# Kernel tuning notes

Hardware: AMD Instinct MI355X
Metric: run time of the kernel (lower is better)

## Reference

```python
import jax, jax.numpy as jnp
import numpy as np

B, L, DH = 4, 4096, 1024
T, DG = 1024, 768
P = 256


def setup_inputs() -> dict:
    key = jax.random.key(0)
    k1, k2, k3, k4, k5 = jax.random.split(key, 5)
    H = jax.random.normal(k1, (B, L, DH), dtype=jnp.float32)
    G = jax.random.normal(k2, (B, T, DG), dtype=jnp.float32)
    # key mask: True = padded/masked. Guarantee at least one valid key per row.
    mask = jax.random.randint(k3, (B, L), 0, 2).astype(jnp.bool_)
    mask = mask.at[:, 0].set(False)
    # torch Linear weights: [out, in]
    Wk_w = jax.random.normal(k4, (P, DH), dtype=jnp.float32) * (DH ** -0.5)
    Wq_w = jax.random.normal(k5, (P, DG), dtype=jnp.float32) * (DG ** -0.5)
    return {"H": H, "G": G, "mask": mask, "Wk_w": Wk_w, "Wq_w": Wq_w}


def reference(H, G, mask, Wk_w, Wq_w):
    # K = Wk(H): [B,L,P]; Q = Wq(G): [B,T,P]
    K = jnp.einsum('bld,pd->blp', H, Wk_w)
    Q = jnp.einsum('btd,pd->btp', G, Wq_w)
    scale = P ** -0.5
    logits = jnp.einsum('btp,blp->btl', Q, K) * scale  # [B,T,L]
    neg_inf = jnp.finfo(logits.dtype).min
    logits = jnp.where(mask[:, None, :], neg_inf, logits)
    alpha = jax.nn.softmax(logits, axis=-1)  # softmax over L (streaming-equivalent)
    Z = jnp.einsum('btl,bld->btd', alpha, H)  # [B,T,DH]
    return Z
```

## Files before the change

### kernel.cpp

```cpp
#include <hip/hip_runtime.h>
#include <hip/hip_bf16.h>


typedef __attribute__((ext_vector_type(8))) short short8;
typedef __attribute__((ext_vector_type(4))) float f32x4;

static __device__ __forceinline__ unsigned short bf16bits(float x) {
    __hip_bfloat16 b = __float2bfloat16(x);
    return *(unsigned short*)&b;
}

static __device__ __forceinline__ void gload_lds16(const __hip_bfloat16* g,
                                                   __hip_bfloat16* l)
{
    auto gp = (const __attribute__((address_space(1))) unsigned int*)(uintptr_t)g;
    auto lp = (__attribute__((address_space(3))) unsigned int*)(unsigned int)(uintptr_t)l;
    __builtin_amdgcn_global_load_lds(gp, lp, 16, 0, 0);
}

__global__ __launch_bounds__(256)
void cvt_f32_bf16_kernel(const float* __restrict__ in,
                         unsigned short* __restrict__ out, int n4)
{
    const int i = blockIdx.x * 256 + threadIdx.x;
    if (i >= n4) return;
    float4 v = ((const float4*)in)[i];
    ushort4 o;
    o.x = bf16bits(v.x); o.y = bf16bits(v.y);
    o.z = bf16bits(v.z); o.w = bf16bits(v.w);
    ((ushort4*)out)[i] = o;
}

__global__ __launch_bounds__(256)
void h_prep_kernel(const float* __restrict__ H,
                   __hip_bfloat16* __restrict__ Hbf,
                   __hip_bfloat16* __restrict__ Ht, int L, int D)
{
    const long b = blockIdx.z;
    const float* Hb = H + b * (long)L * D;
    __hip_bfloat16* Hbfb = Hbf + b * (long)L * D;
    __hip_bfloat16* Htb  = Ht  + b * (long)D * L;
    __shared__ __align__(16) __hip_bfloat16 tile[64][72];
    const int l0 = blockIdx.x * 64, d0 = blockIdx.y * 64;
    const int tx = threadIdx.x & 15, ty = threadIdx.x >> 4;
    #pragma unroll
    for (int p = 0; p < 4; ++p) {
        const int row = ty + p * 16;
        const float4 v = *(const float4*)(&Hb[(long)(l0 + row) * D + d0 + tx * 4]);
        ushort4 o;
        o.x = bf16bits(v.x); o.y = bf16bits(v.y);
        o.z = bf16bits(v.z); o.w = bf16bits(v.w);
        *(ushort4*)(&Hbfb[(long)(l0 + row) * D + d0 + tx * 4]) = o;
        tile[tx * 4 + 0][row] = __float2bfloat16(v.x);
        tile[tx * 4 + 1][row] = __float2bfloat16(v.y);
        tile[tx * 4 + 2][row] = __float2bfloat16(v.z);
        tile[tx * 4 + 3][row] = __float2bfloat16(v.w);
    }
    __syncthreads();
    const int ll = threadIdx.x & 7;
    const int dq = threadIdx.x >> 3;
    #pragma unroll
    for (int q = 0; q < 2; ++q) {
        const int dd = dq + q * 32;
        const short8 v = *(const short8*)(&tile[dd][ll * 8]);
        *(short8*)(&Htb[(long)(d0 + dd) * L + l0 + ll * 8]) = v;
    }
}

template <typename OutT, int SPLITK, int MODE>
__global__ __launch_bounds__(256)
void gemm_bt_kernel(const __hip_bfloat16* __restrict__ A,
                    const __hip_bfloat16* __restrict__ Bm,
                    OutT* __restrict__ C,
                    int K, int lda, int ldb, int ldc,
                    long batchStrideA, long batchStrideB, long batchStrideC,
                    float scale,
                    const unsigned char* __restrict__ mask,
                    const int* __restrict__ widthPtr,
                    float* __restrict__ rowsum,
                    int rowsumStride,
                    long partStride)
{
    int bx = blockIdx.x, by = blockIdx.y, bz = blockIdx.z;
    {
        const int nwg = gridDim.x * gridDim.y * gridDim.z;
        if ((nwg & 7) == 0) {
            int lin = bx + gridDim.x * (by + gridDim.y * bz);
            lin = (lin & 7) * (nwg >> 3) + (lin >> 3);
            bx = lin % gridDim.x;
            const int t = lin / gridDim.x;
            by = t % gridDim.y;
            bz = t / gridDim.y;
        }
    }

    const int zb = bz / SPLITK;
    const int kc = bz % SPLITK;
    A  += (long)zb * batchStrideA;
    Bm += (long)zb * batchStrideB;
    C  += (long)zb * batchStrideC + (long)kc * partStride;
    const int Kloc  = K / SPLITK;
    const int kbase = kc * Kloc;
    const int NT    = Kloc / 32;

    const int tid  = threadIdx.x;
    const int lane = tid & 63;
    const int wave = tid >> 6;
    const int wm = (wave & 1) * 64;
    const int wn = (wave >> 1) * 64;
    const int rowBase = bx * 128;
    const int colBase = by * 128;

    __shared__ __align__(16) __hip_bfloat16 lds_pool[24576];
    __hip_bfloat16* AsP = lds_pool;
    __hip_bfloat16* BsP = lds_pool + 12288;

    f32x4 acc[4][4];
    #pragma unroll
    for (int i = 0; i < 4; ++i)
        #pragma unroll
        for (int j = 0; j < 4; ++j)
            acc[i][j] = (f32x4){0.f, 0.f, 0.f, 0.f};

    const int srow = lane >> 2;
    const int scol = ((lane & 3) ^ ((lane >> 3) & 3)) * 8;
    const long ar0 = (long)(rowBase + wave * 32 + srow) * lda;
    const long ar1 = ar0 + 16l * lda;
    const long br0 = (long)(colBase + wave * 32 + srow) * ldb;
    const long br1 = br0 + 16l * ldb;

    const int mrow = lane & 15;
    const int koff = (((lane >> 4) ^ ((lane >> 1) & 3)) * 8);

    auto stage = [&](int buf, int t) {
        const int kk = kbase + t * 32 + scol;
        gload_lds16(A  + ar0 + kk, AsP + buf * 4096 + wave * 1024);
        gload_lds16(A  + ar1 + kk, AsP + buf * 4096 + wave * 1024 + 512);
        gload_lds16(Bm + br0 + kk, BsP + buf * 4096 + wave * 1024);
        gload_lds16(Bm + br1 + kk, BsP + buf * 4096 + wave * 1024 + 512);
    };

    stage(0, 0);
    if (NT > 1) stage(1, 1);

    int cur = 0;
    for (int t = 0; t < NT; ++t) {
        if (t + 1 < NT)
            asm volatile("s_waitcnt vmcnt(4)" ::: "memory");
        else
            asm volatile("s_waitcnt vmcnt(0)" ::: "memory");
        __builtin_amdgcn_s_barrier();
        if (t + 2 < NT) {
            const int nxt2 = (cur >= 1) ? cur - 1 : cur + 2;
            stage(nxt2, t + 2);
        }

        short8 af[4], bf[4];
        #pragma unroll
        for (int mi = 0; mi < 4; ++mi)
            af[mi] = *(const short8*)(AsP + cur * 4096 + (wm + mi * 16 + mrow) * 32 + koff);
        #pragma unroll
        for (int ni = 0; ni < 4; ++ni)
            bf[ni] = *(const short8*)(BsP + cur * 4096 + (wn + ni * 16 + mrow) * 32 + koff);

        #pragma unroll
        for (int mi = 0; mi < 4; ++mi)
            #pragma unroll
            for (int ni = 0; ni < 4; ++ni)
                acc[mi][ni] = __builtin_amdgcn_mfma_f32_16x16x32_bf16(
                    af[mi], bf[ni], acc[mi][ni], 0, 0, 0);
        cur = (cur == 2) ? 0 : cur + 1;
    }

    const int crow0 = (lane >> 4) * 4;
    const int ccol  = lane & 15;

    if constexpr (MODE == 2 || sizeof(OutT) == 2) {
        __syncthreads();
        __hip_bfloat16* cst = lds_pool;

        if constexpr (MODE == 2) {
            const int w = *widthPtr;
            const long mbase = (long)zb * ldc;
            bool mk[4];
            #pragma unroll
            for (int ni = 0; ni < 4; ++ni) {
                const long midx = mbase + colBase + wn + ni * 16 + ccol;
                if (w == 1)      mk[ni] = mask[midx] != 0;
                else if (w == 2) mk[ni] = ((const unsigned short*)mask)[midx] != 0;
                else if (w == 4) mk[ni] = ((const unsigned int*)mask)[midx] != 0;
                else { uint2 q = ((const uint2*)mask)[midx]; mk[ni] = (q.x | q.y) != 0; }
            }
            #pragma unroll
            for (int mi = 0; mi < 4; ++mi) {
                #pragma unroll
                for (int r = 0; r < 4; ++r) {
                    const int row = wm + mi * 16 + crow0 + r;
                    float rs = 0.f;
                    #pragma unroll
                    for (int ni = 0; ni < 4; ++ni) {
                        const int col = wn + ni * 16 + ccol;
                        const float e = mk[ni] ? 0.f
                                               : __expf(acc[mi][ni][r] * scale);
                        const __hip_bfloat16 pb = __float2bfloat16(e);
                        cst[row * 136 + (((col >> 3) ^ (row >> 3)) << 3) + (col & 7)] = pb;
                        rs += __bfloat162float(pb);
                    }
                    rs += __shfl_xor(rs, 1, 64);
                    rs += __shfl_xor(rs, 2, 64);
                    rs += __shfl_xor(rs, 4, 64);
                    rs += __shfl_xor(rs, 8, 64);
                    if ((lane & 15) == 0)
                        atomicAdd(&rowsum[(long)zb * rowsumStride + rowBase + row], rs);
                }
            }
        } else {
            #pragma unroll
            for (int mi = 0; mi < 4; ++mi) {
                #pragma unroll
                for (int ni = 0; ni < 4; ++ni) {
                    #pragma unroll
                    for (int r = 0; r < 4; ++r) {
                        const int row = wm + mi * 16 + crow0 + r;
                        const int col = wn + ni * 16 + ccol;
                        cst[row * 136 + (((col >> 3) ^ (row >> 3)) << 3) + (col & 7)] =
                            __float2bfloat16(acc[mi][ni][r] * scale);
                    }
                }
            }
        }
        __syncthreads();
        const int g   = tid & 15;
        const int r4  = tid >> 4;
        const int lof = ((g ^ r4) << 3);
        #pragma unroll
        for (int k = 0; k < 8; ++k) {
            const int row = r4 * 8 + k;
            const short8 v = *(const short8*)(cst + row * 136 + lof);
            *(short8*)(&((__hip_bfloat16*)C)[(long)(rowBase + row) * ldc + colBase + g * 8]) = v;
        }
    } else {
        #pragma unroll
        for (int mi = 0; mi < 4; ++mi) {
            #pragma unroll
            for (int ni = 0; ni < 4; ++ni) {
                #pragma unroll
                for (int r = 0; r < 4; ++r) {
                    const int row = rowBase + wm + mi * 16 + crow0 + r;
                    const int col = colBase + wn + ni * 16 + ccol;
                    ((float*)C)[(long)row * ldc + col] = acc[mi][ni][r] * scale;
                }
            }
        }
    }
}

__global__ __launch_bounds__(256)
void combine_kernel(const float* __restrict__ Zp,
                    const float* __restrict__ rowsum,
                    float* __restrict__ Z, long partStride)
{
    const int i = blockIdx.x * 256 + threadIdx.x;
    const float4 a = ((const float4*)Zp)[i];
    const float4 b = ((const float4*)(Zp + partStride))[i];
    const float inv = 1.0f / rowsum[i >> 8];
    float4 o;
    o.x = (a.x + b.x) * inv;
    o.y = (a.y + b.y) * inv;
    o.z = (a.z + b.z) * inv;
    o.w = (a.w + b.w) * inv;
    ((float4*)Z)[i] = o;
}

__global__ __launch_bounds__(256)
void mask_width_kernel(const unsigned char* __restrict__ m, int* __restrict__ widthOut)
{
    __shared__ int c1, c2, c4, c8, cp;
    if (threadIdx.x == 0) { c1 = c2 = c4 = c8 = cp = 0; }
    __syncthreads();
    int l1 = 0, l2 = 0, l4 = 0, l8 = 0, lp = 0;
    const unsigned short* m16 = (const unsigned short*)m;
    const unsigned int*   m32 = (const unsigned int*)m;
    for (int i = threadIdx.x; i < 16384; i += 256) l1 += (m[i] != 0);
    for (int i = threadIdx.x; i < 8192;  i += 256) {
        l2 += (m16[i] != 0);
        lp += ((m[2 * i] != 0) == (m[2 * i + 1] != 0));
    }
    for (int i = threadIdx.x; i < 4096;  i += 256) l4 += (m32[i] != 0);
    for (int i = threadIdx.x; i < 2048;  i += 256) l8 += ((m32[2 * i] | m32[2 * i + 1]) != 0);
    atomicAdd(&c1, l1); atomicAdd(&c2, l2); atomicAdd(&c4, l4);
    atomicAdd(&c8, l8); atomicAdd(&cp, lp);
    __syncthreads();
    if (threadIdx.x == 0) {
        const float f1 = fabsf(c1 / 16384.f - 0.5f);
        const float f2 = fabsf(c2 / 8192.f  - 0.5f);
        const float f4 = fabsf(c4 / 4096.f  - 0.5f);
        const float f8 = fabsf(c8 / 2048.f  - 0.5f);
        int w = 1; float best = f1;
        if (f2 < best) { best = f2; w = 2; }
        if (f4 < best) { best = f4; w = 4; }
        if (f8 < best) { best = f8; w = 8; }
        if (w == 1 && cp > 7400) w = 2;
        *widthOut = w;
    }
}

extern "C" void kernel_launch(void* const* d_in, const int* in_sizes, int n_in,
                              void* d_out, int out_size, void* d_ws, size_t ws_size,
                              hipStream_t stream)
{
    constexpr int B = 4, L = 4096, DH = 1024, T = 1024, DG = 768, P = 256;

    const float* H  = (const float*)d_in[0];
    const float* G  = (const float*)d_in[1];
    const void*  mask = d_in[2];
    const float* Wk = (const float*)d_in[3];
    const float* Wq = (const float*)d_in[4];
    for (int i = 0; i < n_in; ++i) {
        switch (in_sizes[i]) {
            case B * L * DH: H    = (const float*)d_in[i]; break;
            case B * T * DG: G    = (const float*)d_in[i]; break;
            case B * L:      mask = d_in[i];               break;
            case P * DH:     Wk   = (const float*)d_in[i]; break;
            case P * DG:     Wq   = (const float*)d_in[i]; break;
        }
    }
    float* Z = (float*)d_out;

    char* ws = (char*)d_ws;
    __hip_bfloat16* Hbf  = (__hip_bfloat16*)ws;
    float*          Zp   = (float*)ws;
    __hip_bfloat16* Ht   = (__hip_bfloat16*)(ws + (32l << 20));
    __hip_bfloat16* Gbf  = (__hip_bfloat16*)(ws + (64l << 20));
    __hip_bfloat16* Qbf  = (__hip_bfloat16*)(ws + (70l << 20));
    __hip_bfloat16* Kbf  = (__hip_bfloat16*)(ws + (72l << 20));
    __hip_bfloat16* Wkbf = (__hip_bfloat16*)(ws + (80l << 20));
    __hip_bfloat16* Wqbf = (__hip_bfloat16*)(ws + (80l << 20) + (512l << 10));
    float*          rowsum    = (float*)(ws + (80l << 20) + (896l << 10));
    int*            widthFlag = (int*)  (ws + (80l << 20) + (960l << 10));
    __hip_bfloat16* Sb   = (__hip_bfloat16*)(ws + (81l << 20));

    constexpr long ZPART = (long)B * T * DH;

    const dim3 blk(256);

    hipMemsetAsync(rowsum, 0, (size_t)(B * T) * sizeof(float), stream);

    mask_width_kernel<<<dim3(1), blk, 0, stream>>>((const unsigned char*)mask, widthFlag);

    h_prep_kernel<<<dim3(L / 64, DH / 64, B), blk, 0, stream>>>(H, Hbf, Ht, L, DH);
    cvt_f32_bf16_kernel<<<dim3((P * DH) / 1024), blk, 0, stream>>>(Wk, (unsigned short*)Wkbf, (P * DH) / 4);
    cvt_f32_bf16_kernel<<<dim3((P * DG) / 1024), blk, 0, stream>>>(Wq, (unsigned short*)Wqbf, (P * DG) / 4);
    cvt_f32_bf16_kernel<<<dim3((B * T * DG) / 1024), blk, 0, stream>>>(G, (unsigned short*)Gbf, (B * T * DG) / 4);

    gemm_bt_kernel<__hip_bfloat16, 1, 0><<<dim3((B * T) / 128, P / 128, 1), blk, 0, stream>>>(
        Gbf, Wqbf, Qbf, DG, DG, DG, P, 0, 0, 0, 1.0f,
        nullptr, nullptr, nullptr, 0, 0);
    gemm_bt_kernel<__hip_bfloat16, 1, 0><<<dim3((B * L) / 128, P / 128, 1), blk, 0, stream>>>(
        Hbf, Wkbf, Kbf, DH, DH, DH, P, 0, 0, 0, 1.0f,
        nullptr, nullptr, nullptr, 0, 0);
    gemm_bt_kernel<__hip_bfloat16, 1, 2><<<dim3(T / 128, L / 128, B), blk, 0, stream>>>(
        Qbf, Kbf, Sb, P, P, P, L,
        (long)T * P, (long)L * P, (long)T * L, 0.0625f,
        (const unsigned char*)mask, widthFlag, rowsum, T, 0);
    gemm_bt_kernel<float, 2, 0><<<dim3(T / 128, DH / 128, B * 2), blk, 0, stream>>>(
        Sb, Ht, Zp, L, L, L, DH,
        (long)T * L, (long)DH * L, (long)T * DH, 1.0f,
        nullptr, nullptr, nullptr, 0, ZPART);
    combine_kernel<<<dim3((B * T * DH / 4) / 256), blk, 0, stream>>>(
        Zp, rowsum, Z, ZPART);
}
```

Before: 254.6 us.

## Compact unmasked keys per batch and skip masked work in all GEMMs

Adds a mask scan kernel that builds, for each batch, a compacted list of unmasked key indices and a padded count. H is gathered into compacted bf16 and transposed buffers, and the K projection, QK^T/exp and alpha*H GEMMs skip tiles or shorten K past the padded valid count. With about half the keys masked, this roughly halves the work on the large L dimension. The cost is an extra scan launch, gathered loads in h_prep, and dependence on runtime counts. Split-K chunking now depends on lcpad being divisible by 64.

```diff
diff --git a/kernel.cpp b/kernel.cpp
--- a/kernel.cpp
+++ b/kernel.cpp
@@ -32,25 +32,118 @@
 }
 
 __global__ __launch_bounds__(256)
+void mask_width_kernel(const unsigned char* __restrict__ m, int* __restrict__ widthOut)
+{
+    __shared__ int c1, c2, c4, c8, cp;
+    if (threadIdx.x == 0) { c1 = c2 = c4 = c8 = cp = 0; }
+    __syncthreads();
+    int l1 = 0, l2 = 0, l4 = 0, l8 = 0, lp = 0;
+    const unsigned short* m16 = (const unsigned short*)m;
+    const unsigned int*   m32 = (const unsigned int*)m;
+    for (int i = threadIdx.x; i < 16384; i += 256) l1 += (m[i] != 0);
+    for (int i = threadIdx.x; i < 8192;  i += 256) {
+        l2 += (m16[i] != 0);
+        lp += ((m[2 * i] != 0) == (m[2 * i + 1] != 0));
+    }
+    for (int i = threadIdx.x; i < 4096;  i += 256) l4 += (m32[i] != 0);
+    for (int i = threadIdx.x; i < 2048;  i += 256) l8 += ((m32[2 * i] | m32[2 * i + 1]) != 0);
+    atomicAdd(&c1, l1); atomicAdd(&c2, l2); atomicAdd(&c4, l4);
+    atomicAdd(&c8, l8); atomicAdd(&cp, lp);
+    __syncthreads();
+    if (threadIdx.x == 0) {
+        const float f1 = fabsf(c1 / 16384.f - 0.5f);
+        const float f2 = fabsf(c2 / 8192.f  - 0.5f);
+        const float f4 = fabsf(c4 / 4096.f  - 0.5f);
+        const float f8 = fabsf(c8 / 2048.f  - 0.5f);
+        int w = 1; float best = f1;
+        if (f2 < best) { best = f2; w = 2; }
+        if (f4 < best) { best = f4; w = 4; }
+        if (f8 < best) { best = f8; w = 8; }
+        if (w == 1 && cp > 7400) w = 2;
+        *widthOut = w;
+    }
+}
+
+__global__ __launch_bounds__(256)
+void mask_scan_kernel(const void* __restrict__ mask, const int* __restrict__ widthPtr,
+                      unsigned short* __restrict__ idx,
+                      int* __restrict__ lc, int* __restrict__ lcpad, int L)
+{
+    const int b = blockIdx.x;
+    const int tid = threadIdx.x;
+    const int w = *widthPtr;
+    const unsigned char*  m8  = (const unsigned char*)mask;
+    const unsigned short* m16 = (const unsigned short*)mask;
+    const unsigned int*   m32 = (const unsigned int*)mask;
+    const uint2*          m64 = (const uint2*)mask;
+
+    bool v[16];
+    int cnt = 0;
+    #pragma unroll
+    for (int i = 0; i < 16; ++i) {
+        const int l = tid * 16 + i;
+        const long mi = (long)b * L + l;
+        bool masked;
+        if (w == 1)      masked = m8[mi] != 0;
+        else if (w == 2) masked = m16[mi] != 0;
+        else if (w == 4) masked = m32[mi] != 0;
+        else             { uint2 q = m64[mi]; masked = (q.x | q.y) != 0; }
+        v[i] = !masked;
+        cnt += v[i] ? 1 : 0;
+    }
+    __shared__ int waveTot[4];
+    int pre = cnt;
+    #pragma unroll
+    for (int off = 1; off < 64; off <<= 1) {
+        const int t = __shfl_up(pre, off, 64);
+        if ((tid & 63) >= off) pre += t;
+    }
+    if ((tid & 63) == 63) waveTot[tid >> 6] = pre;
+    __syncthreads();
+    int waveOff = 0;
+    for (int wv = 0; wv < (tid >> 6); ++wv) waveOff += waveTot[wv];
+    int o = waveOff + pre - cnt;
+    #pragma unroll
+    for (int i = 0; i < 16; ++i)
+        if (v[i]) idx[(long)b * L + (o++)] = (unsigned short)(tid * 16 + i);
+    if (tid == 255) {
+        const int total = waveOff + pre;
+        lc[b] = total;
+        lcpad[b] = (total + 127) & ~127;
+    }
+}
+
+__global__ __launch_bounds__(256)
 void h_prep_kernel(const float* __restrict__ H,
                    __hip_bfloat16* __restrict__ Hbf,
-                   __hip_bfloat16* __restrict__ Ht, int L, int D)
-{
-    const long b = blockIdx.z;
-    const float* Hb = H + b * (long)L * D;
-    __hip_bfloat16* Hbfb = Hbf + b * (long)L * D;
-    __hip_bfloat16* Htb  = Ht  + b * (long)D * L;
+                   __hip_bfloat16* __restrict__ Ht,
+                   const unsigned short* __restrict__ idx,
+                   const int* __restrict__ lc, const int* __restrict__ lcpad,
+                   int L, int D)
+{
+    const int b = blockIdx.z;
+    const int c0 = blockIdx.x * 64;
+    if (c0 >= lcpad[b]) return;
+    const int Lcb = lc[b];
+    const float* Hb = H + (long)b * L * D;
+    __hip_bfloat16* Hbfb = Hbf + (long)b * L * D;
+    __hip_bfloat16* Htb  = Ht  + (long)b * D * L;
     __shared__ __align__(16) __hip_bfloat16 tile[64][72];
-    const int l0 = blockIdx.x * 64, d0 = blockIdx.y * 64;
+    const int d0 = blockIdx.y * 64;
     const int tx = threadIdx.x & 15, ty = threadIdx.x >> 4;
     #pragma unroll
     for (int p = 0; p < 4; ++p) {
         const int row = ty + p * 16;
-        const float4 v = *(const float4*)(&Hb[(long)(l0 + row) * D + d0 + tx * 4]);
+        const int c = c0 + row;
+        float4 v = {0.f, 0.f, 0.f, 0.f};
+        if (c < Lcb) {
+            const int l = idx[(long)b * L + c];
+            v = *(const float4*)(&Hb[(long)l * D + d0 + tx * 4]);
+        }
         ushort4 o;
         o.x = bf16bits(v.x); o.y = bf16bits(v.y);
         o.z = bf16bits(v.z); o.w = bf16bits(v.w);
-        *(ushort4*)(&Hbfb[(long)(l0 + row) * D + d0 + tx * 4]) = o;
+        *(ushort4*)(&Hbfb[(long)c * D + d0 + tx * 4]) = o;
         tile[tx * 4 + 0][row] = __float2bfloat16(v.x);
         tile[tx * 4 + 1][row] = __float2bfloat16(v.y);
         tile[tx * 4 + 2][row] = __float2bfloat16(v.z);
@@ -63,11 +156,11 @@
     for (int q = 0; q < 2; ++q) {
         const int dd = dq + q * 32;
         const short8 v = *(const short8*)(&tile[dd][ll * 8]);
-        *(short8*)(&Htb[(long)(d0 + dd) * L + l0 + ll * 8]) = v;
-    }
-}
-
-template <typename OutT, int SPLITK, int MODE>
+        *(short8*)(&Htb[(long)(d0 + dd) * L + c0 + ll * 8]) = v;
+    }
+}
+
+template <typename OutT, int SPLITK, int MODE, int CMODE>
 __global__ __launch_bounds__(256)
 void gemm_bt_kernel(const __hip_bfloat16* __restrict__ A,
                     const __hip_bfloat16* __restrict__ Bm,
@@ -75,11 +168,12 @@
                     int K, int lda, int ldb, int ldc,
                     long batchStrideA, long batchStrideB, long batchStrideC,
                     float scale,
-                    const unsigned char* __restrict__ mask,
-                    const int* __restrict__ widthPtr,
                     float* __restrict__ rowsum,
                     int rowsumStride,
-                    long partStride)
+                    long partStride,
+                    const int* __restrict__ lc,
+                    const int* __restrict__ lcpad,
+                    int Lfull)
 {
     int bx = blockIdx.x, by = blockIdx.y, bz = blockIdx.z;
     {
@@ -96,10 +190,23 @@
 
     const int zb = bz / SPLITK;
     const int kc = bz % SPLITK;
+    const int rowBase = bx * 128;
+    const int colBase = by * 128;
+
+    if constexpr (CMODE == 1) {
+        const int bb = rowBase / Lfull;
+        if (rowBase - bb * Lfull >= lcpad[bb]) return;
+    }
+    if constexpr (CMODE == 2) {
+        if (colBase >= lcpad[zb]) return;
+    }
+
     A  += (long)zb * batchStrideA;
     Bm += (long)zb * batchStrideB;
     C  += (long)zb * batchStrideC + (long)kc * partStride;
-    const int Kloc  = K / SPLITK;
+    int Kdyn = K;
+    if constexpr (CMODE == 3) Kdyn = lcpad[zb];
+    const int Kloc  = Kdyn / SPLITK;
     const int kbase = kc * Kloc;
     const int NT    = Kloc / 32;
 
@@ -108,8 +215,6 @@
     const int wave = tid >> 6;
     const int wm = (wave & 1) * 64;
     const int wn = (wave >> 1) * 64;
-    const int rowBase = bx * 128;
-    const int colBase = by * 128;
 
     __shared__ __align__(16) __hip_bfloat16 lds_pool[24576];
     __hip_bfloat16* AsP = lds_pool;
@@ -180,17 +285,11 @@
         __hip_bfloat16* cst = lds_pool;
 
         if constexpr (MODE == 2) {
-            const int w = *widthPtr;
-            const long mbase = (long)zb * ldc;
+            const int lcv = lc[zb];
             bool mk[4];
             #pragma unroll
-            for (int ni = 0; ni < 4; ++ni) {
-                const long midx = mbase + colBase + wn + ni * 16 + ccol;
-                if (w == 1)      mk[ni] = mask[midx] != 0;
-                else if (w == 2) mk[ni] = ((const unsigned short*)mask)[midx] != 0;
-                else if (w == 4) mk[ni] = ((const unsigned int*)mask)[midx] != 0;
-                else { uint2 q = ((const uint2*)mask)[midx]; mk[ni] = (q.x | q.y) != 0; }
-            }
+            for (int ni = 0; ni < 4; ++ni)
+                mk[ni] = (colBase + wn + ni * 16 + ccol) >= lcv;
             #pragma unroll
             for (int mi = 0; mi < 4; ++mi) {
                 #pragma unroll
@@ -272,39 +371,6 @@
     ((float4*)Z)[i] = o;
 }
 
-__global__ __launch_bounds__(256)
-void mask_width_kernel(const unsigned char* __restrict__ m, int* __restrict__ widthOut)
-{
-    __shared__ int c1, c2, c4, c8, cp;
-    if (threadIdx.x == 0) { c1 = c2 = c4 = c8 = cp = 0; }
-    __syncthreads();
-    int l1 = 0, l2 = 0, l4 = 0, l8 = 0, lp = 0;
-    const unsigned short* m16 = (const unsigned short*)m;
-    const unsigned int*   m32 = (const unsigned int*)m;
-    for (int i = threadIdx.x; i < 16384; i += 256) l1 += (m[i] != 0);
-    for (int i = threadIdx.x; i < 8192;  i += 256) {
-        l2 += (m16[i] != 0);
-        lp += ((m[2 * i] != 0) == (m[2 * i + 1] != 0));
-    }
-    for (int i = threadIdx.x; i < 4096;  i += 256) l4 += (m32[i] != 0);
-    for (int i = threadIdx.x; i < 2048;  i += 256) l8 += ((m32[2 * i] | m32[2 * i + 1]) != 0);
-    atomicAdd(&c1, l1); atomicAdd(&c2, l2); atomicAdd(&c4, l4);
-    atomicAdd(&c8, l8); atomicAdd(&cp, lp);
-    __syncthreads();
-    if (threadIdx.x == 0) {
-        const float f1 = fabsf(c1 / 16384.f - 0.5f);
-        const float f2 = fabsf(c2 / 8192.f  - 0.5f);
-        const float f4 = fabsf(c4 / 4096.f  - 0.5f);
-        const float f8 = fabsf(c8 / 2048.f  - 0.5f);
-        int w = 1; float best = f1;
-        if (f2 < best) { best = f2; w = 2; }
-        if (f4 < best) { best = f4; w = 4; }
-        if (f8 < best) { best = f8; w = 8; }
-        if (w == 1 && cp > 7400) w = 2;
-        *widthOut = w;
-    }
-}
-
 extern "C" void kernel_launch(void* const* d_in, const int* in_sizes, int n_in,
                               void* d_out, int out_size, void* d_ws, size_t ws_size,
                               hipStream_t stream)
@@ -338,6 +404,9 @@
     __hip_bfloat16* Wqbf = (__hip_bfloat16*)(ws + (80l << 20) + (512l << 10));
     float*          rowsum    = (float*)(ws + (80l << 20) + (896l << 10));
     int*            widthFlag = (int*)  (ws + (80l << 20) + (960l << 10));
+    int*            lcBuf     = (int*)  (ws + (80l << 20) + (961l << 10));
+    int*            lcpadBuf  = (int*)  (ws + (80l << 20) + (961l << 10) + 64);
+    unsigned short* idxBuf    = (unsigned short*)(ws + (80l << 20) + (962l << 10));
     __hip_bfloat16* Sb   = (__hip_bfloat16*)(ws + (81l << 20));
 
     constexpr long ZPART = (long)B * T * DH;
@@ -347,26 +416,28 @@
     hipMemsetAsync(rowsum, 0, (size_t)(B * T) * sizeof(float), stream);
 
     mask_width_kernel<<<dim3(1), blk, 0, stream>>>((const unsigned char*)mask, widthFlag);
-
-    h_prep_kernel<<<dim3(L / 64, DH / 64, B), blk, 0, stream>>>(H, Hbf, Ht, L, DH);
+    mask_scan_kernel<<<dim3(B), blk, 0, stream>>>(mask, widthFlag, idxBuf, lcBuf, lcpadBuf, L);
+
+    h_prep_kernel<<<dim3(L / 64, DH / 64, B), blk, 0, stream>>>(
+        H, Hbf, Ht, idxBuf, lcBuf, lcpadBuf, L, DH);
     cvt_f32_bf16_kernel<<<dim3((P * DH) / 1024), blk, 0, stream>>>(Wk, (unsigned short*)Wkbf, (P * DH) / 4);
     cvt_f32_bf16_kernel<<<dim3((P * DG) / 1024), blk, 0, stream>>>(Wq, (unsigned short*)Wqbf, (P * DG) / 4);
     cvt_f32_bf16_kernel<<<dim3((B * T * DG) / 1024), blk, 0, stream>>>(G, (unsigned short*)Gbf, (B * T * DG) / 4);
 
-    gemm_bt_kernel<__hip_bfloat16, 1, 0><<<dim3((B * T) / 128, P / 128, 1), blk, 0, stream>>>(
+    gemm_bt_kernel<__hip_bfloat16, 1, 0, 0><<<dim3((B * T) / 128, P / 128, 1), blk, 0, stream>>>(
         Gbf, Wqbf, Qbf, DG, DG, DG, P, 0, 0, 0, 1.0f,
-        nullptr, nullptr, nullptr, 0, 0);
-    gemm_bt_kernel<__hip_bfloat16, 1, 0><<<dim3((B * L) / 128, P / 128, 1), blk, 0, stream>>>(
+        nullptr, 0, 0, nullptr, nullptr, 0);
+    gemm_bt_kernel<__hip_bfloat16, 1, 0, 1><<<dim3((B * L) / 128, P / 128, 1), blk, 0, stream>>>(
         Hbf, Wkbf, Kbf, DH, DH, DH, P, 0, 0, 0, 1.0f,
-        nullptr, nullptr, nullptr, 0, 0);
-    gemm_bt_kernel<__hip_bfloat16, 1, 2><<<dim3(T / 128, L / 128, B), blk, 0, stream>>>(
+        nullptr, 0, 0, nullptr, lcpadBuf, L);
+    gemm_bt_kernel<__hip_bfloat16, 1, 2, 2><<<dim3(T / 128, L / 128, B), blk, 0, stream>>>(
         Qbf, Kbf, Sb, P, P, P, L,
         (long)T * P, (long)L * P, (long)T * L, 0.0625f,
-        (const unsigned char*)mask, widthFlag, rowsum, T, 0);
-    gemm_bt_kernel<float, 2, 0><<<dim3(T / 128, DH / 128, B * 2), blk, 0, stream>>>(
+        rowsum, T, 0, lcBuf, lcpadBuf, L);
+    gemm_bt_kernel<float, 2, 0, 3><<<dim3(T / 128, DH / 128, B * 2), blk, 0, stream>>>(
         Sb, Ht, Zp, L, L, L, DH,
         (long)T * L, (long)DH * L, (long)T * DH, 1.0f,
-        nullptr, nullptr, nullptr, 0, ZPART);
+        nullptr, 0, ZPART, nullptr, lcpadBuf, L);
     combine_kernel<<<dim3((B * T * DH / 4) / 256), blk, 0, stream>>>(
         Zp, rowsum, Z, ZPART);
 }
```

New measurement: 239.8 us. 1.06x faster.
